# Kernel tuning notes

Hardware: AMD Instinct MI355X
Metric: run time of the kernel (lower is better)

Reference implementation:

```python
import jax, jax.numpy as jnp
import numpy as np

N = 50000       # nodes
E = 800000      # directed edges (src -> dst)
INDIM, HID, OUT = 256, 128, 64
NEG_SLOPE = 0.2  # PyG GATConv default negative_slope


def gat_layer(x, src, dst, W, a_src, a_dst, b, n_nodes):
    """Single-head PyG-style GATConv with self-loops already in (src, dst)."""
    h = x @ W.T                                   # [N, F_out]
    alpha_src = h @ a_src                         # [N]
    alpha_dst = h @ a_dst                         # [N]
    # per-edge attention logits, LeakyReLU
    e = jax.nn.leaky_relu(alpha_src[src] + alpha_dst[dst], NEG_SLOPE)  # [E']
    # segment softmax grouped by destination node (numerically stable)
    m = jnp.full((n_nodes,), -jnp.inf, e.dtype).at[dst].max(e)
    ee = jnp.exp(e - m[dst])
    denom = jax.ops.segment_sum(ee, dst, num_segments=n_nodes)
    alpha = ee / denom[dst]                       # [E']
    # weighted scatter-add of source messages
    out = jax.ops.segment_sum(h[src] * alpha[:, None], dst, num_segments=n_nodes)
    return out + b


def setup_inputs() -> dict:
    key = jax.random.key(0)
    ks = jax.random.split(key, 10)
    s = 0.1
    return {
        "x": jax.random.normal(ks[0], (N, INDIM), jnp.float32),
        "edge_index": jax.random.randint(ks[1], (2, E), 0, N, dtype=jnp.int32),
        "W1": jax.random.normal(ks[2], (HID, INDIM), jnp.float32) * s,
        "a_src1": jax.random.normal(ks[3], (HID,), jnp.float32) * s,
        "a_dst1": jax.random.normal(ks[4], (HID,), jnp.float32) * s,
        "b1": jnp.zeros((HID,), jnp.float32),
        "W2": jax.random.normal(ks[5], (OUT, HID), jnp.float32) * s,
        "a_src2": jax.random.normal(ks[6], (OUT,), jnp.float32) * s,
        "a_dst2": jax.random.normal(ks[7], (OUT,), jnp.float32) * s,
        "b2": jnp.zeros((OUT,), jnp.float32),
    }


def reference(x, edge_index, W1, a_src1, a_dst1, b1, W2, a_src2, a_dst2, b2):
    n_nodes = x.shape[0]
    # PyG GATConv default add_self_loops=True
    loops = jnp.arange(n_nodes, dtype=edge_index.dtype)
    src = jnp.concatenate([edge_index[0], loops])
    dst = jnp.concatenate([edge_index[1], loops])
    h = gat_layer(x, src, dst, W1, a_src1, a_dst1, b1, n_nodes)
    h = jax.nn.relu(h)
    h = gat_layer(h, src, dst, W2, a_src2, a_dst2, b2, n_nodes)
    return h
```

## Files before the change

### kernel.cpp

```cpp
#include <hip/hip_runtime.h>
#include <hip/hip_bf16.h>
#include <math.h>

#define NN 50000
#define EE 800000
#define INDIM 256
#define HID 128
#define OUTF 64
#define NEG_SLOPE 0.2f
#define CAP 64

#define NB ((NN + 255) >> 8)
#define BCAP 6144
#define CHUNK 2048
#define EPT 8

typedef __attribute__((ext_vector_type(8))) short bf16x8;
typedef __attribute__((ext_vector_type(4))) float f32x4;

__device__ inline float bflo(unsigned p) { return __uint_as_float(p << 16); }
__device__ inline float bfhi(unsigned p) { return __uint_as_float(p & 0xffff0000u); }
__device__ inline unsigned f2bf(float f) {
    unsigned u = __float_as_uint(f);
    return (u + 0x7fffu + ((u >> 16) & 1u)) >> 16;
}
__device__ inline float leaky(float l) { return (l > 0.f) ? l : NEG_SLOPE * l; }

template <typename AT, int BN, int WR, int WC, bool FA, bool FAL>
__device__ inline void gemm_body(const AT* __restrict__ A,
                                 const float* __restrict__ B,
                                 unsigned short* __restrict__ Cb,
                                 const float* __restrict__ a_s,
                                 const float* __restrict__ a_d,
                                 float* __restrict__ asrc,
                                 float* __restrict__ adst,
                                 int N, int K, int bid)
{
    constexpr int BM = 128, LD = 40;
    constexpr int MF = (BM / WR) / 16;
    constexpr int NF = (BN / WC) / 16;
    static_assert(!FA || WC == 1, "register alpha needs full cols per wave");
    __shared__ unsigned short As[BM * LD];
    __shared__ unsigned short Bs[BN * LD];
    __shared__ float al_s[FAL ? 2 * BM : 2];

    const int tid = threadIdx.x;
    const int wave = tid >> 6, lane = tid & 63;
    const int wr = wave / WC, wc = wave % WC;
    const int wrow0 = wr * (BM / WR);
    const int wcol0 = wc * (BN / WC);
    const int row0 = bid * BM;
    const int lrow = lane & 15, lkg = lane >> 4;

    if constexpr (FAL) {
        for (int i = tid; i < 2 * BM; i += 256) al_s[i] = 0.f;
    }

    f32x4 acc[MF][NF];
    #pragma unroll
    for (int mi = 0; mi < MF; ++mi)
        #pragma unroll
        for (int ni = 0; ni < NF; ++ni) acc[mi][ni] = 0.f;

    for (int k0 = 0; k0 < K; k0 += 32) {
        if constexpr (sizeof(AT) == 4) {
            #pragma unroll
            for (int i = tid; i < BM * 8; i += 256) {
                int row = i >> 3, kq = i & 7;
                float4 v = make_float4(0.f, 0.f, 0.f, 0.f);
                int gr = row0 + row;
                if (gr < N) v = *(const float4*)((const float*)A + (size_t)gr * K + k0 + kq * 4);
                unsigned p0 = f2bf(v.x) | (f2bf(v.y) << 16);
                unsigned p1 = f2bf(v.z) | (f2bf(v.w) << 16);
                *(uint2*)&As[row * LD + kq * 4] = make_uint2(p0, p1);
            }
        } else {
            #pragma unroll
            for (int i = tid; i < BM * 4; i += 256) {
                int row = i >> 2, q = i & 3;
                uint4 v = make_uint4(0u, 0u, 0u, 0u);
                int gr = row0 + row;
                if (gr < N) v = *(const uint4*)((const unsigned short*)A + (size_t)gr * K + k0 + q * 8);
                *(uint4*)&As[row * LD + q * 8] = v;
            }
        }
        #pragma unroll
        for (int i = tid; i < BN * 8; i += 256) {
            int row = i >> 3, kq = i & 7;
            float4 v = *(const float4*)(B + (size_t)row * K + k0 + kq * 4);
            unsigned p0 = f2bf(v.x) | (f2bf(v.y) << 16);
            unsigned p1 = f2bf(v.z) | (f2bf(v.w) << 16);
            *(uint2*)&Bs[row * LD + kq * 4] = make_uint2(p0, p1);
        }
        __syncthreads();

        bf16x8 af[MF], bfr[NF];
        #pragma unroll
        for (int mi = 0; mi < MF; ++mi)
            af[mi] = *(const bf16x8*)&As[(wrow0 + mi * 16 + lrow) * LD + lkg * 8];
        #pragma unroll
        for (int ni = 0; ni < NF; ++ni)
            bfr[ni] = *(const bf16x8*)&Bs[(wcol0 + ni * 16 + lrow) * LD + lkg * 8];
        #pragma unroll
        for (int mi = 0; mi < MF; ++mi)
            #pragma unroll
            for (int ni = 0; ni < NF; ++ni)
                acc[mi][ni] = __builtin_amdgcn_mfma_f32_16x16x32_bf16(
                    af[mi], bfr[ni], acc[mi][ni], 0, 0, 0);
        __syncthreads();
    }

    if constexpr (FA || FAL) {
        float asv[NF], adv[NF];
        #pragma unroll
        for (int ni = 0; ni < NF; ++ni) {
            int c = wcol0 + ni * 16 + lrow;
            asv[ni] = a_s[c]; adv[ni] = a_d[c];
        }
        #pragma unroll
        for (int mi = 0; mi < MF; ++mi)
            #pragma unroll
            for (int r = 0; r < 4; ++r) {
                float ps = 0.f, pd = 0.f;
                #pragma unroll
                for (int ni = 0; ni < NF; ++ni) {
                    ps = fmaf(acc[mi][ni][r], asv[ni], ps);
                    pd = fmaf(acc[mi][ni][r], adv[ni], pd);
                }
                #pragma unroll
                for (int d = 1; d < 16; d <<= 1) {
                    ps += __shfl_xor(ps, d);
                    pd += __shfl_xor(pd, d);
                }
                int lr_ = wrow0 + mi * 16 + lkg * 4 + r;
                if constexpr (FA) {
                    int gr = row0 + lr_;
                    if (lrow == 0 && gr < N) { asrc[gr] = ps; adst[gr] = pd; }
                } else {
                    if (lrow == 0) {
                        atomicAdd(&al_s[lr_], ps);
                        atomicAdd(&al_s[BM + lr_], pd);
                    }
                }
            }
    }

    #pragma unroll
    for (int mi = 0; mi < MF; ++mi)
        #pragma unroll
        for (int ni = 0; ni < NF; ++ni)
            #pragma unroll
            for (int r = 0; r < 4; ++r) {
                int gr = row0 + wrow0 + mi * 16 + lkg * 4 + r;
                int gc = wcol0 + ni * 16 + lrow;
                if (gr < N)
                    Cb[(size_t)gr * BN + gc] = (unsigned short)f2bf(acc[mi][ni][r]);
            }

    if constexpr (FAL) {
        __syncthreads();
        if (tid < BM) {
            int gr = row0 + tid;
            if (gr < N) { asrc[gr] = al_s[tid]; adst[gr] = al_s[BM + tid]; }
        }
    }
}

__device__ inline void bin_body(int bb,
                                const int* __restrict__ src_in,
                                const int* __restrict__ dst_in,
                                unsigned* __restrict__ gbucket,
                                int* __restrict__ bcnt,
                                int E, int tot)
{
    __shared__ int h_hist[256];
    __shared__ int h_scan[256];
    __shared__ int h_ofs[256];
    __shared__ int h_gbase[256];
    __shared__ unsigned grp[CHUNK];

    const int tid = threadIdx.x;
    const int e0 = bb * CHUNK;
    const int cntc = min(CHUNK, tot - e0);

    h_hist[tid] = 0;
    __syncthreads();

    unsigned pk[EPT];
    bool val[EPT];
    #pragma unroll
    for (int u = 0; u < EPT; ++u) {
        int e = e0 + u * 256 + tid;
        val[u] = (e < tot);
        if (val[u]) {
            int d, s;
            if (e < E) { d = dst_in[e]; s = src_in[e]; }
            else       { d = e - E;    s = d; }
            pk[u] = ((unsigned)d << 16) | (unsigned)s;
            atomicAdd(&h_hist[d >> 8], 1);
        }
    }
    __syncthreads();

    int v = h_hist[tid];
    int incl = v;
    h_scan[tid] = incl;
    __syncthreads();
    for (int off = 1; off < 256; off <<= 1) {
        int t = (tid >= off) ? h_scan[tid - off] : 0;
        __syncthreads();
        incl += t;
        h_scan[tid] = incl;
        __syncthreads();
    }
    int excl = incl - v;
    h_scan[tid] = excl;
    h_ofs[tid] = excl;
    h_gbase[tid] = (tid < NB && v > 0) ? atomicAdd(&bcnt[tid], v) : 0;
    __syncthreads();

    #pragma unroll
    for (int u = 0; u < EPT; ++u)
        if (val[u]) {
            int b = pk[u] >> 24;
            int pos = atomicAdd(&h_ofs[b], 1);
            grp[pos] = pk[u];
        }
    __syncthreads();

    for (int i = tid; i < cntc; i += 256) {
        unsigned p = grp[i];
        int b = p >> 24;
        int gp = h_gbase[b] + (i - h_scan[b]);
        if (gp < BCAP) gbucket[(size_t)b * BCAP + gp] = p;
    }
}

__global__ __launch_bounds__(256) void fused_gemm1_bin(
    const float* __restrict__ x, const float* __restrict__ W1,
    unsigned short* __restrict__ h1b,
    const float* __restrict__ a_s, const float* __restrict__ a_d,
    float* __restrict__ asrc, float* __restrict__ adst,
    const int* __restrict__ src_in, const int* __restrict__ dst_in,
    unsigned* __restrict__ gbucket, int* __restrict__ bcnt,
    int N, int K, int GB, int E)
{
    if ((int)blockIdx.x < GB) {
        gemm_body<float, 128, 2, 2, false, true>(x, W1, h1b, a_s, a_d,
                                                 asrc, adst, N, K, blockIdx.x);
    } else {
        bin_body(blockIdx.x - GB, src_in, dst_in, gbucket, bcnt, E, E + N);
    }
}

__global__ __launch_bounds__(256) void csr_build(
    const unsigned* __restrict__ gbucket, const int* __restrict__ bcnt,
    int* __restrict__ cnt, unsigned short* __restrict__ csr, int N)
{
    __shared__ int c2[256];
    __shared__ unsigned short cl[256 * CAP];

    const int b = blockIdx.x;
    const int tid = threadIdx.x;
    c2[tid] = 0;
    __syncthreads();

    int len = bcnt[b];
    if (len > BCAP) len = BCAP;
    for (int i = tid; i < len; i += 256) {
        unsigned p = gbucket[(size_t)b * BCAP + i];
        int dl = (p >> 16) & 255;
        int s  = p & 0xffff;
        int r = atomicAdd(&c2[dl], 1);
        if (r < CAP) cl[(dl << 6) + r] = (unsigned short)s;
    }
    __syncthreads();

    int d = (b << 8) + tid;
    if (d < N) cnt[d] = c2[tid];

    int rows = N - (b << 8);
    rows = (rows > 256) ? 256 : rows;
    const uint4* sp = (const uint4*)cl;
    uint4* dp = (uint4*)(csr + (((size_t)b << 8) << 6));
    for (int i = tid; i < rows * 8; i += 256) dp[i] = sp[i];
}

__global__ __launch_bounds__(256) void gemm2_alpha_kernel(
    const unsigned short* __restrict__ A, const float* __restrict__ B,
    unsigned short* __restrict__ Cb,
    const float* __restrict__ a_s, const float* __restrict__ a_d,
    float* __restrict__ asrc, float* __restrict__ adst, int N, int K)
{
    gemm_body<unsigned short, 64, 4, 1, true, false>(A, B, Cb, a_s, a_d,
                                                     asrc, adst, N, K, blockIdx.x);
}

template <int F, bool RELU, bool OUTBF>
__global__ __launch_bounds__(256) void aggregate_kernel(
    const unsigned short* __restrict__ hb, const unsigned short* __restrict__ csr,
    const int* __restrict__ cnt_arr, const float* __restrict__ asrc,
    const float* __restrict__ adst, const float* __restrict__ bias,
    void* __restrict__ outv, int n)
{
    constexpr int G = F / 8;
    constexpr int EPI = 64 / G;
    constexpr int STEP = EPI * 4;
    int wave = (int)((blockIdx.x * (size_t)blockDim.x + threadIdx.x) >> 6);
    int lane = threadIdx.x & 63;
    if (wave >= n) return;
    const size_t beg = (size_t)wave << 6;
    int cntv = cnt_arr[wave];
    cntv = (cntv > CAP) ? CAP : cntv;
    const float ad = adst[wave];
    const int grp = lane / G, fl = lane % G;

    float acc[8];
    #pragma unroll
    for (int p = 0; p < 8; ++p) acc[p] = 0.f;

    int s = 0;
    float e = 0.f;
    if (lane < cntv) { s = (int)csr[beg + lane]; e = __expf(leaky(asrc[s] + ad)); }
    float denom = e;
    #pragma unroll
    for (int d = 32; d > 0; d >>= 1) denom += __shfl_xor(denom, d);
    float w = e * __fdividef(1.f, denom);

    for (int jj0 = 0; jj0 < cntv; jj0 += STEP) {
        uint4 q[4];
        float wj[4];
        #pragma unroll
        for (int u = 0; u < 4; ++u) {
            int sel = jj0 + u * EPI + grp;
            int sj = __shfl(s, sel);
            wj[u] = __shfl(w, sel);
            q[u] = make_uint4(0u, 0u, 0u, 0u);
            if (sel < cntv)
                q[u] = *(const uint4*)(hb + (size_t)sj * F + fl * 8);
        }
        #pragma unroll
        for (int u = 0; u < 4; ++u) {
            acc[0] += wj[u] * bflo(q[u].x); acc[1] += wj[u] * bfhi(q[u].x);
            acc[2] += wj[u] * bflo(q[u].y); acc[3] += wj[u] * bfhi(q[u].y);
            acc[4] += wj[u] * bflo(q[u].z); acc[5] += wj[u] * bfhi(q[u].z);
            acc[6] += wj[u] * bflo(q[u].w); acc[7] += wj[u] * bfhi(q[u].w);
        }
    }

    #pragma unroll
    for (int d = G; d < 64; d <<= 1)
        #pragma unroll
        for (int p = 0; p < 8; ++p) acc[p] += __shfl_xor(acc[p], d);

    if (lane < G) {
        float v[8];
        #pragma unroll
        for (int p = 0; p < 8; ++p) {
            v[p] = acc[p] + bias[fl * 8 + p];
            if (RELU) v[p] = fmaxf(v[p], 0.f);
        }
        if constexpr (OUTBF) {
            unsigned short* o = (unsigned short*)outv + (size_t)wave * F + fl * 8;
            uint4 pk;
            pk.x = f2bf(v[0]) | (f2bf(v[1]) << 16);
            pk.y = f2bf(v[2]) | (f2bf(v[3]) << 16);
            pk.z = f2bf(v[4]) | (f2bf(v[5]) << 16);
            pk.w = f2bf(v[6]) | (f2bf(v[7]) << 16);
            *(uint4*)o = pk;
        } else {
            float* o = (float*)outv + (size_t)wave * F + fl * 8;
            *(float4*)o       = make_float4(v[0], v[1], v[2], v[3]);
            *(float4*)(o + 4) = make_float4(v[4], v[5], v[6], v[7]);
        }
    }
}

extern "C" void kernel_launch(void* const* d_in, const int* in_sizes, int n_in,
                              void* d_out, int out_size, void* d_ws, size_t ws_size,
                              hipStream_t stream)
{
    const float* x      = (const float*)d_in[0];
    const int*   ei     = (const int*)d_in[1];
    const float* W1     = (const float*)d_in[2];
    const float* a_src1 = (const float*)d_in[3];
    const float* a_dst1 = (const float*)d_in[4];
    const float* b1     = (const float*)d_in[5];
    const float* W2     = (const float*)d_in[6];
    const float* a_src2 = (const float*)d_in[7];
    const float* a_dst2 = (const float*)d_in[8];
    const float* b2     = (const float*)d_in[9];
    float* out = (float*)d_out;

    const int N = NN, E = EE;
    const int* src_in = ei;
    const int* dst_in = ei + E;

    char* p = (char*)d_ws;
    unsigned short* h1b   = (unsigned short*)p; p += (size_t)N * HID * 2;
    unsigned short* hmidb = (unsigned short*)p; p += (size_t)N * HID * 2;
    unsigned short* h2b   = (unsigned short*)p; p += (size_t)N * OUTF * 2;
    float* asrc = (float*)p; p += (size_t)N * 4;
    float* adst = (float*)p; p += (size_t)N * 4;
    int* cnt    = (int*)p;   p += (size_t)N * 4;
    unsigned short* csr = (unsigned short*)p; p += (size_t)N * CAP * 2;
    int* bcnt = (int*)p; p += 256 * 4;
    unsigned* gbucket = (unsigned*)h2b;

    hipMemsetAsync(bcnt, 0, 256 * 4, stream);

    const int GB   = (N + 127) / 128;
    const int BINB = (E + N + CHUNK - 1) / CHUNK;
    const int nwb  = (N * 64 + 255) / 256;

    fused_gemm1_bin<<<GB + BINB, 256, 0, stream>>>(
        x, W1, h1b, a_src1, a_dst1, asrc, adst, src_in, dst_in,
        gbucket, bcnt, N, INDIM, GB, E);
    csr_build<<<NB, 256, 0, stream>>>(gbucket, bcnt, cnt, csr, N);

    aggregate_kernel<HID, true, true><<<nwb, 256, 0, stream>>>(
        h1b, csr, cnt, asrc, adst, b1, hmidb, N);

    gemm2_alpha_kernel<<<GB, 256, 0, stream>>>(hmidb, W2, h2b, a_src2, a_dst2,
                                               asrc, adst, N, HID);
    aggregate_kernel<OUTF, false, false><<<nwb, 256, 0, stream>>>(
        h2b, csr, cnt, asrc, adst, b2, out, N);

    (void)in_sizes; (void)n_in; (void)out_size; (void)ws_size;
}
```

Before: 221.7 us.

## Split fused gemm1/bin kernel, prefetch GEMM tiles via registers, pad bucket counters

The GEMM main loop now loads the next K-slice of A and B into registers while MFMAs run on the current LDS tile, so global-load latency overlaps compute. The heterogeneous fused gemm1+binning kernel is split back into separate bin, csr_build and gemm1 launches. The per-bucket atomic counters are padded apart to avoid contention on shared cache lines. The split adds a launch and gives up the concurrency between GEMM and binning blocks, and the prefetch raises register pressure.

```diff
diff --git a/kernel.cpp b/kernel.cpp
--- a/kernel.cpp
+++ b/kernel.cpp
@@ -14,6 +14,7 @@
 #define BCAP 6144
 #define CHUNK 2048
 #define EPT 8
+#define BPAD 16
 
 typedef __attribute__((ext_vector_type(8))) short bf16x8;
 typedef __attribute__((ext_vector_type(4))) float f32x4;
@@ -39,6 +40,8 @@
     constexpr int BM = 128, LD = 40;
     constexpr int MF = (BM / WR) / 16;
     constexpr int NF = (BN / WC) / 16;
+    constexpr int NA  = (sizeof(AT) == 4) ? (BM * 8 / 256) : (BM * 4 / 256);
+    constexpr int NBL = BN * 8 / 256;
     static_assert(!FA || WC == 1, "register alpha needs full cols per wave");
     __shared__ unsigned short As[BM * LD];
     __shared__ unsigned short Bs[BN * LD];
@@ -56,43 +59,68 @@
         for (int i = tid; i < 2 * BM; i += 256) al_s[i] = 0.f;
     }
 
-    f32x4 acc[MF][NF];
-    #pragma unroll
-    for (int mi = 0; mi < MF; ++mi)
-        #pragma unroll
-        for (int ni = 0; ni < NF; ++ni) acc[mi][ni] = 0.f;
-
-    for (int k0 = 0; k0 < K; k0 += 32) {
+    int arow[NA], aoff[NA]; bool aval[NA];
+    #pragma unroll
+    for (int u = 0; u < NA; ++u) {
+        int i = u * 256 + tid;
+        if constexpr (sizeof(AT) == 4) { arow[u] = i >> 3; aoff[u] = (i & 7) * 4; }
+        else                           { arow[u] = i >> 2; aoff[u] = (i & 3) * 8; }
+        aval[u] = (row0 + arow[u]) < N;
+    }
+    int brow[NBL], boff[NBL];
+    #pragma unroll
+    for (int u = 0; u < NBL; ++u) {
+        int i = u * 256 + tid;
+        brow[u] = i >> 3; boff[u] = (i & 7) * 4;
+    }
+
+    uint4 ra[NA], rb[NBL];
+    auto loadA = [&](int k0) {
+        #pragma unroll
+        for (int u = 0; u < NA; ++u) {
+            ra[u] = make_uint4(0u, 0u, 0u, 0u);
+            if (aval[u])
+                ra[u] = *(const uint4*)((const AT*)A + (size_t)(row0 + arow[u]) * K + k0 + aoff[u]);
+        }
+    };
+    auto loadB = [&](int k0) {
+        #pragma unroll
+        for (int u = 0; u < NBL; ++u)
+            rb[u] = *(const uint4*)(B + (size_t)brow[u] * K + k0 + boff[u]);
+    };
+    auto storeLDS = [&]() {
         if constexpr (sizeof(AT) == 4) {
             #pragma unroll
-            for (int i = tid; i < BM * 8; i += 256) {
-                int row = i >> 3, kq = i & 7;
-                float4 v = make_float4(0.f, 0.f, 0.f, 0.f);
-                int gr = row0 + row;
-                if (gr < N) v = *(const float4*)((const float*)A + (size_t)gr * K + k0 + kq * 4);
-                unsigned p0 = f2bf(v.x) | (f2bf(v.y) << 16);
-                unsigned p1 = f2bf(v.z) | (f2bf(v.w) << 16);
-                *(uint2*)&As[row * LD + kq * 4] = make_uint2(p0, p1);
+            for (int u = 0; u < NA; ++u) {
+                unsigned p0 = f2bf(__uint_as_float(ra[u].x)) | (f2bf(__uint_as_float(ra[u].y)) << 16);
+                unsigned p1 = f2bf(__uint_as_float(ra[u].z)) | (f2bf(__uint_as_float(ra[u].w)) << 16);
+                *(uint2*)&As[arow[u] * LD + aoff[u]] = make_uint2(p0, p1);
             }
         } else {
             #pragma unroll
-            for (int i = tid; i < BM * 4; i += 256) {
-                int row = i >> 2, q = i & 3;
-                uint4 v = make_uint4(0u, 0u, 0u, 0u);
-                int gr = row0 + row;
-                if (gr < N) v = *(const uint4*)((const unsigned short*)A + (size_t)gr * K + k0 + q * 8);
-                *(uint4*)&As[row * LD + q * 8] = v;
-            }
-        }
-        #pragma unroll
-        for (int i = tid; i < BN * 8; i += 256) {
-            int row = i >> 3, kq = i & 7;
-            float4 v = *(const float4*)(B + (size_t)row * K + k0 + kq * 4);
-            unsigned p0 = f2bf(v.x) | (f2bf(v.y) << 16);
-            unsigned p1 = f2bf(v.z) | (f2bf(v.w) << 16);
-            *(uint2*)&Bs[row * LD + kq * 4] = make_uint2(p0, p1);
-        }
+            for (int u = 0; u < NA; ++u)
+                *(uint4*)&As[arow[u] * LD + aoff[u]] = ra[u];
+        }
+        #pragma unroll
+        for (int u = 0; u < NBL; ++u) {
+            unsigned p0 = f2bf(__uint_as_float(rb[u].x)) | (f2bf(__uint_as_float(rb[u].y)) << 16);
+            unsigned p1 = f2bf(__uint_as_float(rb[u].z)) | (f2bf(__uint_as_float(rb[u].w)) << 16);
+            *(uint2*)&Bs[brow[u] * LD + boff[u]] = make_uint2(p0, p1);
+        }
+    };
+
+    f32x4 acc[MF][NF];
+    #pragma unroll
+    for (int mi = 0; mi < MF; ++mi)
+        #pragma unroll
+        for (int ni = 0; ni < NF; ++ni) acc[mi][ni] = 0.f;
+
+    const int NK = K / 32;
+    loadA(0); loadB(0);
+    for (int ks = 0; ks < NK; ++ks) {
+        storeLDS();
         __syncthreads();
+        if (ks + 1 < NK) { loadA((ks + 1) * 32); loadB((ks + 1) * 32); }
 
         bf16x8 af[MF], bfr[NF];
         #pragma unroll
@@ -166,12 +194,30 @@
     }
 }
 
-__device__ inline void bin_body(int bb,
-                                const int* __restrict__ src_in,
-                                const int* __restrict__ dst_in,
-                                unsigned* __restrict__ gbucket,
-                                int* __restrict__ bcnt,
-                                int E, int tot)
+__global__ __launch_bounds__(256) void gemm1_kernel(
+    const float* __restrict__ x, const float* __restrict__ W1,
+    unsigned short* __restrict__ h1b,
+    const float* __restrict__ a_s, const float* __restrict__ a_d,
+    float* __restrict__ asrc, float* __restrict__ adst, int N, int K)
+{
+    gemm_body<float, 128, 2, 2, false, true>(x, W1, h1b, a_s, a_d,
+                                             asrc, adst, N, K, blockIdx.x);
+}
+
+__global__ __launch_bounds__(256) void gemm2_alpha_kernel(
+    const unsigned short* __restrict__ A, const float* __restrict__ B,
+    unsigned short* __restrict__ Cb,
+    const float* __restrict__ a_s, const float* __restrict__ a_d,
+    float* __restrict__ asrc, float* __restrict__ adst, int N, int K)
+{
+    gemm_body<unsigned short, 64, 4, 1, true, false>(A, B, Cb, a_s, a_d,
+                                                     asrc, adst, N, K, blockIdx.x);
+}
+
+__global__ __launch_bounds__(256) void bin_kernel(
+    const int* __restrict__ src_in, const int* __restrict__ dst_in,
+    unsigned* __restrict__ gbucket, int* __restrict__ bcnt,
+    int E, int tot)
 {
     __shared__ int h_hist[256];
     __shared__ int h_scan[256];
@@ -180,7 +226,7 @@
     __shared__ unsigned grp[CHUNK];
 
     const int tid = threadIdx.x;
-    const int e0 = bb * CHUNK;
+    const int e0 = blockIdx.x * CHUNK;
     const int cntc = min(CHUNK, tot - e0);
 
     h_hist[tid] = 0;
@@ -216,7 +262,7 @@
     int excl = incl - v;
     h_scan[tid] = excl;
     h_ofs[tid] = excl;
-    h_gbase[tid] = (tid < NB && v > 0) ? atomicAdd(&bcnt[tid], v) : 0;
+    h_gbase[tid] = (tid < NB && v > 0) ? atomicAdd(&bcnt[tid * BPAD], v) : 0;
     __syncthreads();
 
     #pragma unroll
@@ -236,23 +282,6 @@
     }
 }
 
-__global__ __launch_bounds__(256) void fused_gemm1_bin(
-    const float* __restrict__ x, const float* __restrict__ W1,
-    unsigned short* __restrict__ h1b,
-    const float* __restrict__ a_s, const float* __restrict__ a_d,
-    float* __restrict__ asrc, float* __restrict__ adst,
-    const int* __restrict__ src_in, const int* __restrict__ dst_in,
-    unsigned* __restrict__ gbucket, int* __restrict__ bcnt,
-    int N, int K, int GB, int E)
-{
-    if ((int)blockIdx.x < GB) {
-        gemm_body<float, 128, 2, 2, false, true>(x, W1, h1b, a_s, a_d,
-                                                 asrc, adst, N, K, blockIdx.x);
-    } else {
-        bin_body(blockIdx.x - GB, src_in, dst_in, gbucket, bcnt, E, E + N);
-    }
-}
-
 __global__ __launch_bounds__(256) void csr_build(
     const unsigned* __restrict__ gbucket, const int* __restrict__ bcnt,
     int* __restrict__ cnt, unsigned short* __restrict__ csr, int N)
@@ -265,7 +294,7 @@
     c2[tid] = 0;
     __syncthreads();
 
-    int len = bcnt[b];
+    int len = bcnt[b * BPAD];
     if (len > BCAP) len = BCAP;
     for (int i = tid; i < len; i += 256) {
         unsigned p = gbucket[(size_t)b * BCAP + i];
@@ -284,16 +313,6 @@
     const uint4* sp = (const uint4*)cl;
     uint4* dp = (uint4*)(csr + (((size_t)b << 8) << 6));
     for (int i = tid; i < rows * 8; i += 256) dp[i] = sp[i];
-}
-
-__global__ __launch_bounds__(256) void gemm2_alpha_kernel(
-    const unsigned short* __restrict__ A, const float* __restrict__ B,
-    unsigned short* __restrict__ Cb,
-    const float* __restrict__ a_s, const float* __restrict__ a_d,
-    float* __restrict__ asrc, float* __restrict__ adst, int N, int K)
-{
-    gemm_body<unsigned short, 64, 4, 1, true, false>(A, B, Cb, a_s, a_d,
-                                                     asrc, adst, N, K, blockIdx.x);
 }
 
 template <int F, bool RELU, bool OUTBF>
@@ -404,20 +423,20 @@
     float* adst = (float*)p; p += (size_t)N * 4;
     int* cnt    = (int*)p;   p += (size_t)N * 4;
     unsigned short* csr = (unsigned short*)p; p += (size_t)N * CAP * 2;
-    int* bcnt = (int*)p; p += 256 * 4;
+    int* bcnt = (int*)p; p += (size_t)NB * BPAD * 4;
     unsigned* gbucket = (unsigned*)h2b;
 
-    hipMemsetAsync(bcnt, 0, 256 * 4, stream);
+    hipMemsetAsync(bcnt, 0, (size_t)NB * BPAD * 4, stream);
 
     const int GB   = (N + 127) / 128;
     const int BINB = (E + N + CHUNK - 1) / CHUNK;
     const int nwb  = (N * 64 + 255) / 256;
 
-    fused_gemm1_bin<<<GB + BINB, 256, 0, stream>>>(
-        x, W1, h1b, a_src1, a_dst1, asrc, adst, src_in, dst_in,
-        gbucket, bcnt, N, INDIM, GB, E);
+    bin_kernel<<<BINB, 256, 0, stream>>>(src_in, dst_in, gbucket, bcnt, E, E + N);
     csr_build<<<NB, 256, 0, stream>>>(gbucket, bcnt, cnt, csr, N);
 
+    gemm1_kernel<<<GB, 256, 0, stream>>>(x, W1, h1b, a_src1, a_dst1,
+                                         asrc, adst, N, INDIM);
     aggregate_kernel<HID, true, true><<<nwb, 256, 0, stream>>>(
         h1b, csr, cnt, asrc, adst, b1, hmidb, N);
 
```

New measurement: 209.7 us. 1.06x faster.
